# Optimization experiments

Hardware: AMD Instinct MI355X
Metric: run time of the kernel (lower is better)

## Reference

```python
import jax, jax.numpy as jnp
import numpy as np

DIM = 4096
N_HEADS = 32
N_KV_HEADS = 8
HEAD_DIM = DIM // N_HEADS  # 128
N_REP = N_HEADS // N_KV_HEADS  # 4
B, S = 1, 2048
ROPE_THETA = 500000.0


def setup_inputs() -> dict:
    key = jax.random.key(0)
    ks = jax.random.split(key, 5)
    sc = 0.02
    x = jax.random.normal(ks[0], (B, S, DIM), jnp.float32)
    wq = jax.random.normal(ks[1], (DIM, N_HEADS * HEAD_DIM), jnp.float32) * sc
    wk = jax.random.normal(ks[2], (DIM, N_KV_HEADS * HEAD_DIM), jnp.float32) * sc
    wv = jax.random.normal(ks[3], (DIM, N_KV_HEADS * HEAD_DIM), jnp.float32) * sc
    wo = jax.random.normal(ks[4], (N_HEADS * HEAD_DIM, DIM), jnp.float32) * sc
    # rotary frequencies: freqs_cis = exp(i * t * theta^(-2j/d)), j in [0, head_dim/2)
    inv_freq = 1.0 / (ROPE_THETA ** (jnp.arange(0, HEAD_DIM, 2, dtype=jnp.float32) / HEAD_DIM))
    t = jnp.arange(S, dtype=jnp.float32)
    ang = jnp.outer(t, inv_freq)  # (S, head_dim/2)
    freqs_cos = jnp.cos(ang)
    freqs_sin = jnp.sin(ang)
    # additive causal mask, broadcastable to (B, H, S, S)
    mask = jnp.where(jnp.triu(jnp.ones((S, S), bool), k=1), -jnp.inf, 0.0).astype(jnp.float32)[None, None]
    return {"x": x, "wq": wq, "wk": wk, "wv": wv, "wo": wo,
            "freqs_cos": freqs_cos, "freqs_sin": freqs_sin, "mask": mask}


def _apply_rotary(t, cos, sin):
    # t: (B, S, n, hd); complex multiply on consecutive pairs (x0,x1),(x2,x3),...
    b, s, n, hd = t.shape
    tr = t.reshape(b, s, n, hd // 2, 2)
    re, im = tr[..., 0], tr[..., 1]
    c = cos[None, :, None, :]
    sn = sin[None, :, None, :]
    out_re = re * c - im * sn
    out_im = re * sn + im * c
    return jnp.stack([out_re, out_im], axis=-1).reshape(b, s, n, hd)


def reference(x, wq, wk, wv, wo, freqs_cos, freqs_sin, mask):
    b, s, _ = x.shape
    xq = (x @ wq).reshape(b, s, N_HEADS, HEAD_DIM)
    xk = (x @ wk).reshape(b, s, N_KV_HEADS, HEAD_DIM)
    xv = (x @ wv).reshape(b, s, N_KV_HEADS, HEAD_DIM)
    xq = _apply_rotary(xq, freqs_cos, freqs_sin)
    xk = _apply_rotary(xk, freqs_cos, freqs_sin)
    # repeat_kv (GQA): expand kv heads to match query heads
    keys = jnp.repeat(xk, N_REP, axis=2)    # (b, s, H, hd)
    values = jnp.repeat(xv, N_REP, axis=2)
    # (b, H, s, hd)
    q = xq.transpose(0, 2, 1, 3)
    k = keys.transpose(0, 2, 1, 3)
    v = values.transpose(0, 2, 1, 3)
    scores = jnp.einsum('bhqd,bhkd->bhqk', q, k) / np.sqrt(HEAD_DIM).astype(np.float32)
    scores = scores + mask
    probs = jax.nn.softmax(scores.astype(jnp.float32), axis=-1).astype(q.dtype)
    out = jnp.einsum('bhqk,bhkd->bhqd', probs, v)
    out = out.transpose(0, 2, 1, 3).reshape(b, s, N_HEADS * HEAD_DIM)
    return out @ wo
```

## Files before the change

### kernel.cpp

```cpp
#include <hip/hip_runtime.h>
#include <cstdint>
#include <cstddef>

typedef _Float16 f16_t;
typedef f16_t f16x8 __attribute__((ext_vector_type(8)));
typedef float  floatx4 __attribute__((ext_vector_type(4)));

#define S_LEN 2048
#define DIM_  4096
#define NH    32
#define NKV   8
#define HD    128
#define KV_DIM (NKV * HD)
#define QLD   (DIM_ + 2 * KV_DIM)

__device__ __forceinline__ float bf16r(float x) {
    uint32_t u = __float_as_uint(x);
    u = (u + 0x7fffu + ((u >> 16) & 1u)) & 0xffff0000u;
    return __uint_as_float(u);
}

__device__ __forceinline__ void gload_lds16(const f16_t* g, f16_t* l) {
    __builtin_amdgcn_global_load_lds(
        (const __attribute__((address_space(1))) void*)g,
        (__attribute__((address_space(3))) void*)l, 16, 0, 0);
}

__global__ void f32_to_f16_kernel(const float* __restrict__ in,
                                  f16_t* __restrict__ out, int n) {
    int i = (blockIdx.x * blockDim.x + threadIdx.x) * 8;
    if (i >= n) return;
    float4 a = *(const float4*)(in + i);
    float4 b = *(const float4*)(in + i + 4);
    f16x8 o;
    o[0] = (f16_t)bf16r(a.x); o[1] = (f16_t)bf16r(a.y);
    o[2] = (f16_t)bf16r(a.z); o[3] = (f16_t)bf16r(a.w);
    o[4] = (f16_t)bf16r(b.x); o[5] = (f16_t)bf16r(b.y);
    o[6] = (f16_t)bf16r(b.z); o[7] = (f16_t)bf16r(b.w);
    *(f16x8*)(out + i) = o;
}

__global__ void transpose_weights_kernel(const float* __restrict__ wq,
                                         const float* __restrict__ wk,
                                         const float* __restrict__ wv,
                                         const float* __restrict__ wo,
                                         f16_t* __restrict__ wqkvT,
                                         f16_t* __restrict__ woT) {
    __shared__ float tile[32][33];
    int bid = blockIdx.x;
    const float* in; f16_t* out; int C;
    if (bid < 16384)      { in = wq; out = wqkvT;                          C = 4096; }
    else if (bid < 20480) { bid -= 16384; in = wk; out = wqkvT + (size_t)4096 * 4096; C = 1024; }
    else if (bid < 24576) { bid -= 20480; in = wv; out = wqkvT + (size_t)5120 * 4096; C = 1024; }
    else                  { bid -= 24576; in = wo; out = woT;              C = 4096; }
    int gpr = C / 32;
    int bx = (bid % gpr) * 32;
    int by = (bid / gpr) * 32;
    int tx = threadIdx.x, ty = threadIdx.y;
#pragma unroll
    for (int i = 0; i < 4; i++) {
        int r = ty + i * 8;
        tile[r][tx] = in[(size_t)(by + r) * C + bx + tx];
    }
    __syncthreads();
#pragma unroll
    for (int i = 0; i < 4; i++) {
        int r = ty + i * 8;
        out[(size_t)(bx + r) * 4096 + by + tx] = (f16_t)bf16r(tile[tx][r]);
    }
}

__global__ void transpose_f16_kernel(const f16_t* __restrict__ in,
                                     f16_t* __restrict__ out,
                                     int ldi, int ldo) {
    __shared__ float tile[32][33];
    int bx = blockIdx.x * 32;
    int by = blockIdx.y * 32;
    int tx = threadIdx.x, ty = threadIdx.y;
#pragma unroll
    for (int i = 0; i < 4; i++) {
        int r = ty + i * 8;
        tile[r][tx] = (float)in[(size_t)(by + r) * ldi + bx + tx];
    }
    __syncthreads();
#pragma unroll
    for (int i = 0; i < 4; i++) {
        int r = ty + i * 8;
        out[(size_t)(bx + r) * ldo + by + tx] = (f16_t)tile[tx][r];
    }
}

template <int BM, int BN, typename OutT>
__global__ __launch_bounds__(512) void gemm_pipe_kernel(
        const f16_t* __restrict__ A, const f16_t* __restrict__ BT,
        OutT* __restrict__ C, int M, int N, int K, int nbx) {
    constexpr int BK = 32;
    constexpr int WN = BN / 64;
    constexpr int WM = 8 / WN;
    constexpr int MT = BM / WM / 16;
    constexpr int NT = 4;
    constexpr int ABY = BM * BK * 2;
    constexpr int BBY = BN * BK * 2;
    constexpr int AISS = ABY / 8192;
    constexpr int BISS = BBY / 8192;
    constexpr int LOADS = AISS + BISS;
    constexpr int BUF_EL = (ABY + BBY) / 2;

    __shared__ f16_t lds[3 * BUF_EL];

    const int tid  = threadIdx.x;
    const int lane = tid & 63;
    const int wave = tid >> 6;
    const int quad = lane >> 4;
    const int l16  = lane & 15;
    const int wn = (wave % WN) * 64;
    const int wm = (wave / WN) * (BM / WM);

    const int nwg = gridDim.x;
    const int swz = (blockIdx.x & 7) * (nwg >> 3) + (blockIdx.x >> 3);
    const int m0 = (swz / nbx) * BM;
    const int n0 = (swz % nbx) * BN;

    const f16_t* Arow = A  + (size_t)m0 * K;
    const f16_t* Brow = BT + (size_t)n0 * K;
    const int nt_tiles = K / BK;

    floatx4 acc[MT][NT] = {};

    auto stage = [&](int t, int q) {
        const int k0 = t * BK;
        f16_t* LdA = lds + q * BUF_EL;
#pragma unroll
        for (int j = 0; j < AISS; j++) {
            int Lb  = j * 8192 + tid * 16;
            int row = Lb >> 6;
            int cb  = (Lb & 48) ^ (((Lb >> 7) & 3) << 4);
            gload_lds16(Arow + (size_t)row * K + k0 + (cb >> 1), LdA + (Lb >> 1));
        }
        f16_t* LdB = lds + q * BUF_EL + ABY / 2;
#pragma unroll
        for (int j = 0; j < BISS; j++) {
            int Lb  = j * 8192 + tid * 16;
            int row = Lb >> 6;
            int cb  = (Lb & 48) ^ (((Lb >> 7) & 3) << 4);
            gload_lds16(Brow + (size_t)row * K + k0 + (cb >> 1), LdB + (Lb >> 1));
        }
    };

    stage(0, 0);
    stage(1, 1);
    if constexpr (LOADS == 4) asm volatile("s_waitcnt vmcnt(4)" ::: "memory");
    else                      asm volatile("s_waitcnt vmcnt(3)" ::: "memory");
    __builtin_amdgcn_s_barrier();
    __builtin_amdgcn_sched_barrier(0);

    for (int t = 0; t < nt_tiles; ++t) {
        const int cur = t % 3;
        const bool pre = (t + 2 < nt_tiles);
        if (pre) stage(t + 2, (t + 2) % 3);

        const f16_t* Ab = lds + cur * BUF_EL;
        const f16_t* Bb = Ab + ABY / 2;
        f16x8 af[MT], bf[NT];
#pragma unroll
        for (int mt = 0; mt < MT; mt++) {
            int r  = wm + mt * 16 + l16;
            int cb = (quad * 16) ^ (((r >> 1) & 3) << 4);
            af[mt] = *(const f16x8*)(Ab + r * 32 + (cb >> 1));
        }
#pragma unroll
        for (int nt = 0; nt < NT; nt++) {
            int r  = wn + nt * 16 + l16;
            int cb = (quad * 16) ^ (((r >> 1) & 3) << 4);
            bf[nt] = *(const f16x8*)(Bb + r * 32 + (cb >> 1));
        }
        asm volatile("s_waitcnt lgkmcnt(0)" ::: "memory");
        __builtin_amdgcn_sched_barrier(0);
        __builtin_amdgcn_s_setprio(1);
#pragma unroll
        for (int mt = 0; mt < MT; mt++)
#pragma unroll
            for (int nt = 0; nt < NT; nt++)
                acc[mt][nt] = __builtin_amdgcn_mfma_f32_16x16x32_f16(
                    af[mt], bf[nt], acc[mt][nt], 0, 0, 0);
        __builtin_amdgcn_s_setprio(0);
        if (pre) {
            if constexpr (LOADS == 4) asm volatile("s_waitcnt vmcnt(4)" ::: "memory");
            else                      asm volatile("s_waitcnt vmcnt(3)" ::: "memory");
        } else {
            asm volatile("s_waitcnt vmcnt(0)" ::: "memory");
        }
        __builtin_amdgcn_s_barrier();
        __builtin_amdgcn_sched_barrier(0);
    }

#pragma unroll
    for (int mt = 0; mt < MT; mt++)
#pragma unroll
        for (int nt = 0; nt < NT; nt++)
#pragma unroll
            for (int rg = 0; rg < 4; rg++) {
                int row = m0 + wm + mt * 16 + quad * 4 + rg;
                int col = n0 + wn + nt * 16 + l16;
                C[(size_t)row * N + col] = (OutT)acc[mt][nt][rg];
            }
}

__global__ __launch_bounds__(512) void attn_kernel(
        const f16_t* __restrict__ QKV, const f16_t* __restrict__ Vt,
        const float* __restrict__ fcos, const float* __restrict__ fsin,
        f16_t* __restrict__ O) {
    constexpr int BK = 64;
    constexpr int KS = HD + 8;
    constexpr int VS = BK + 8;
    __shared__ f16_t Ks[BK][KS];
    __shared__ f16_t Vs[HD][VS];
    __shared__ f16_t Ps[8][16][72];

    const int tid  = threadIdx.x;
    const int lane = tid & 63;
    const int wave = tid >> 6;
    const int quad = lane >> 4;
    const int l16  = lane & 15;

    const int bid = blockIdx.x;
    const int h   = bid & 31;
    const int g   = bid >> 5;
    const int qt  = (g < 8) ? g : 23 - g;
    const int q0  = qt * 128;
    const int hkv = h >> 2;

    const int qrow = q0 + wave * 16 + l16;
    f16x8 qf[4];
    {
        const f16_t* Qg = QKV + (size_t)qrow * QLD + h * HD;
        const float* cr = fcos + qrow * 64;
        const float* sr = fsin + qrow * 64;
#pragma unroll
        for (int c = 0; c < 4; c++) {
            f16x8 v = *(const f16x8*)(Qg + c * 32 + quad * 8);
#pragma unroll
            for (int u = 0; u < 4; u++) {
                int fi = c * 16 + quad * 4 + u;
                float cc = bf16r(cr[fi]), ss = bf16r(sr[fi]);
                float re = (float)v[2 * u], im = (float)v[2 * u + 1];
                v[2 * u]     = (f16_t)(re * cc - im * ss);
                v[2 * u + 1] = (f16_t)(re * ss + im * cc);
            }
            qf[c] = v;
        }
    }

    floatx4 o_acc[8] = {};
    float m_run[4], l_run[4];
#pragma unroll
    for (int i = 0; i < 4; i++) { m_run[i] = -1e30f; l_run[i] = 0.f; }
    const float scale = 0.08838834764831845f;

    const int q_lo = q0 + wave * 16;
    const int q_hi = q_lo + 15;
    const int ntiles = q0 / BK + 2;

    const int krr = tid >> 4;
    const int kcc = (tid & 15) * 8;
    const int vr  = tid >> 3;
    const int vc  = (tid & 7) * 8;
    const f16_t* Vg = Vt + (size_t)hkv * HD * S_LEN;

    for (int t = 0; t < ntiles; t++) {
        const int k0 = t * BK;

#pragma unroll
        for (int p = 0; p < 2; p++) {
            int krow = k0 + p * 32 + krr;
            f16x8 v = *(const f16x8*)(QKV + (size_t)krow * QLD + DIM_ + hkv * HD + kcc);
            const float* cr = fcos + krow * 64;
            const float* sr = fsin + krow * 64;
#pragma unroll
            for (int u = 0; u < 4; u++) {
                int fi = kcc / 2 + u;
                float cc = bf16r(cr[fi]), ss = bf16r(sr[fi]);
                float re = (float)v[2 * u], im = (float)v[2 * u + 1];
                v[2 * u]     = (f16_t)(re * cc - im * ss);
                v[2 * u + 1] = (f16_t)(re * ss + im * cc);
            }
            *(f16x8*)&Ks[p * 32 + krr][kcc] = v;
        }
#pragma unroll
        for (int p = 0; p < 2; p++)
            *(f16x8*)&Vs[p * 64 + vr][vc] =
                *(const f16x8*)(Vg + (size_t)(p * 64 + vr) * S_LEN + k0 + vc);
        __syncthreads();

        if (k0 <= q_hi) {
            floatx4 sc4[4] = {};
#pragma unroll
            for (int nt = 0; nt < 4; nt++)
#pragma unroll
                for (int ks = 0; ks < 4; ks++) {
                    f16x8 kf = *(const f16x8*)&Ks[nt * 16 + l16][ks * 32 + quad * 8];
                    sc4[nt] = __builtin_amdgcn_mfma_f32_16x16x32_f16(qf[ks], kf, sc4[nt], 0, 0, 0);
                }

            const bool needmask = (k0 + BK - 1) > q_lo;
#pragma unroll
            for (int nt = 0; nt < 4; nt++)
#pragma unroll
                for (int rg = 0; rg < 4; rg++) {
                    float s = sc4[nt][rg] * scale;
                    if (needmask) {
                        int qg = q_lo + quad * 4 + rg;
                        int kg = k0 + nt * 16 + l16;
                        if (kg > qg) s = -1e30f;
                    }
                    sc4[nt][rg] = s;
                }

            float alpha[4];
#pragma unroll
            for (int rg = 0; rg < 4; rg++) {
                float m = fmaxf(fmaxf(sc4[0][rg], sc4[1][rg]), fmaxf(sc4[2][rg], sc4[3][rg]));
#pragma unroll
                for (int off = 8; off >= 1; off >>= 1)
                    m = fmaxf(m, __shfl_xor(m, off, 64));
                float mn = fmaxf(m_run[rg], m);
                alpha[rg] = __expf(m_run[rg] - mn);
                m_run[rg] = mn;
            }
            float rsum[4] = {0.f, 0.f, 0.f, 0.f};
#pragma unroll
            for (int nt = 0; nt < 4; nt++)
#pragma unroll
                for (int rg = 0; rg < 4; rg++) {
                    float p = __expf(sc4[nt][rg] - m_run[rg]);
                    sc4[nt][rg] = p;
                    rsum[rg] += p;
                }
#pragma unroll
            for (int rg = 0; rg < 4; rg++) {
                float s = rsum[rg];
#pragma unroll
                for (int off = 8; off >= 1; off >>= 1)
                    s += __shfl_xor(s, off, 64);
                l_run[rg] = l_run[rg] * alpha[rg] + s;
            }
#pragma unroll
            for (int dt = 0; dt < 8; dt++)
#pragma unroll
                for (int rg = 0; rg < 4; rg++) o_acc[dt][rg] *= alpha[rg];

#pragma unroll
            for (int nt = 0; nt < 4; nt++)
#pragma unroll
                for (int rg = 0; rg < 4; rg++)
                    Ps[wave][quad * 4 + rg][nt * 16 + l16] = (f16_t)sc4[nt][rg];
            asm volatile("s_waitcnt lgkmcnt(0)" ::: "memory");
            __builtin_amdgcn_sched_barrier(0);

#pragma unroll
            for (int ks = 0; ks < 2; ks++) {
                f16x8 pf = *(const f16x8*)&Ps[wave][l16][ks * 32 + quad * 8];
#pragma unroll
                for (int dt = 0; dt < 8; dt++) {
                    f16x8 vf = *(const f16x8*)&Vs[dt * 16 + l16][ks * 32 + quad * 8];
                    o_acc[dt] = __builtin_amdgcn_mfma_f32_16x16x32_f16(pf, vf, o_acc[dt], 0, 0, 0);
                }
            }
        }
        __syncthreads();
    }

#pragma unroll
    for (int rg = 0; rg < 4; rg++) {
        float inv_l = 1.0f / l_run[rg];
#pragma unroll
        for (int dt = 0; dt < 8; dt++) {
            int row = q0 + wave * 16 + quad * 4 + rg;
            int col = h * HD + dt * 16 + l16;
            O[(size_t)row * (NH * HD) + col] = (f16_t)(o_acc[dt][rg] * inv_l);
        }
    }
}

extern "C" void kernel_launch(void* const* d_in, const int* in_sizes, int n_in,
                              void* d_out, int out_size, void* d_ws, size_t ws_size,
                              hipStream_t stream) {
    const float* x    = (const float*)d_in[0];
    const float* wq   = (const float*)d_in[1];
    const float* wk   = (const float*)d_in[2];
    const float* wv   = (const float*)d_in[3];
    const float* wo   = (const float*)d_in[4];
    const float* fcos = (const float*)d_in[5];
    const float* fsin = (const float*)d_in[6];
    float* out = (float*)d_out;

    char* ws = (char*)d_ws;
    constexpr size_t MB = 1024 * 1024;
    f16_t* xb    = (f16_t*)(ws + 0 * MB);
    f16_t* wqkvT = (f16_t*)(ws + 16 * MB);
    f16_t* woT   = (f16_t*)(ws + 64 * MB);
    f16_t* QKVb  = (f16_t*)(ws + 96 * MB);
    f16_t* Vt    = (f16_t*)(ws + 120 * MB);
    f16_t* attnb = (f16_t*)(ws + 124 * MB);

    f32_to_f16_kernel<<<S_LEN * DIM_ / 8 / 256, 256, 0, stream>>>(x, xb, S_LEN * DIM_);
    transpose_weights_kernel<<<40960, dim3(32, 8), 0, stream>>>(wq, wk, wv, wo, wqkvT, woT);

    gemm_pipe_kernel<256, 256, f16_t><<<192, 512, 0, stream>>>(
        xb, wqkvT, QKVb, S_LEN, QLD, DIM_, QLD / 256);

    transpose_f16_kernel<<<dim3(KV_DIM / 32, S_LEN / 32), dim3(32, 8), 0, stream>>>(
        QKVb + 5120, Vt, QLD, S_LEN);

    attn_kernel<<<512, 512, 0, stream>>>(QKVb, Vt, fcos, fsin, attnb);

    gemm_pipe_kernel<256, 128, float><<<256, 512, 0, stream>>>(
        attnb, woT, out, S_LEN, DIM_, DIM_, DIM_ / 128);
}
```

Before: 561.9 us.

## Precompute RoPE in separate pass and streamline attention inner loop

Moves the rotary embedding and softmax scale out of the attention kernel into a standalone pass over the Q and K columns, so the attention loop no longer recomputes RoPE on K for every query tile. K and V tiles are now loaded with direct global-to-LDS loads into an XOR-swizzled layout. The loop rescales the accumulators only when the running max grows by more than a threshold, and computes the row sums with an MFMA against a ones vector instead of shuffle reductions. This adds a kernel launch and an extra read/write of Q and K, and pre-scaling Q and skipping rescales could slightly change fp16 precision.

```diff
diff --git a/kernel.cpp b/kernel.cpp
--- a/kernel.cpp
+++ b/kernel.cpp
@@ -90,6 +90,26 @@
     }
 }
 
+__global__ void rope_qk_kernel(f16_t* __restrict__ QKV,
+                               const float* __restrict__ fcos,
+                               const float* __restrict__ fsin) {
+    int c8 = (blockIdx.x * blockDim.x + threadIdx.x) * 8;
+    int row = blockIdx.y;
+    f16_t* p = QKV + (size_t)row * QLD + c8;
+    f16x8 v = *(f16x8*)p;
+    const float* cr = fcos + row * 64 + ((c8 & 127) >> 1);
+    const float* sr = fsin + row * 64 + ((c8 & 127) >> 1);
+    const float sc = (c8 < DIM_) ? 0.08838834764831845f : 1.0f;
+#pragma unroll
+    for (int u = 0; u < 4; u++) {
+        float cc = bf16r(cr[u]), ss = bf16r(sr[u]);
+        float re = (float)v[2 * u], im = (float)v[2 * u + 1];
+        v[2 * u]     = (f16_t)((re * cc - im * ss) * sc);
+        v[2 * u + 1] = (f16_t)((re * ss + im * cc) * sc);
+    }
+    *(f16x8*)p = v;
+}
+
 template <int BM, int BN, typename OutT>
 __global__ __launch_bounds__(512) void gemm_pipe_kernel(
         const f16_t* __restrict__ A, const f16_t* __restrict__ BT,
@@ -208,13 +228,10 @@
 
 __global__ __launch_bounds__(512) void attn_kernel(
         const f16_t* __restrict__ QKV, const f16_t* __restrict__ Vt,
-        const float* __restrict__ fcos, const float* __restrict__ fsin,
         f16_t* __restrict__ O) {
     constexpr int BK = 64;
-    constexpr int KS = HD + 8;
-    constexpr int VS = BK + 8;
-    __shared__ f16_t Ks[BK][KS];
-    __shared__ f16_t Vs[HD][VS];
+    __shared__ f16_t Ks[BK * HD];
+    __shared__ f16_t Vs[HD * BK];
     __shared__ f16_t Ps[8][16][72];
 
     const int tid  = threadIdx.x;
@@ -231,138 +248,113 @@
     const int hkv = h >> 2;
 
     const int qrow = q0 + wave * 16 + l16;
+    const f16_t* Qg = QKV + (size_t)qrow * QLD + h * HD;
     f16x8 qf[4];
-    {
-        const f16_t* Qg = QKV + (size_t)qrow * QLD + h * HD;
-        const float* cr = fcos + qrow * 64;
-        const float* sr = fsin + qrow * 64;
-#pragma unroll
-        for (int c = 0; c < 4; c++) {
-            f16x8 v = *(const f16x8*)(Qg + c * 32 + quad * 8);
-#pragma unroll
-            for (int u = 0; u < 4; u++) {
-                int fi = c * 16 + quad * 4 + u;
-                float cc = bf16r(cr[fi]), ss = bf16r(sr[fi]);
-                float re = (float)v[2 * u], im = (float)v[2 * u + 1];
-                v[2 * u]     = (f16_t)(re * cc - im * ss);
-                v[2 * u + 1] = (f16_t)(re * ss + im * cc);
-            }
-            qf[c] = v;
-        }
-    }
+#pragma unroll
+    for (int c = 0; c < 4; c++) qf[c] = *(const f16x8*)(Qg + c * 32 + quad * 8);
 
     floatx4 o_acc[8] = {};
-    float m_run[4], l_run[4];
-#pragma unroll
-    for (int i = 0; i < 4; i++) { m_run[i] = -1e30f; l_run[i] = 0.f; }
-    const float scale = 0.08838834764831845f;
+    floatx4 l_acc = {0.f, 0.f, 0.f, 0.f};
+    float m_run[4];
+#pragma unroll
+    for (int i = 0; i < 4; i++) m_run[i] = -1e30f;
+
+    f16x8 ones;
+#pragma unroll
+    for (int i = 0; i < 8; i++) ones[i] = (f16_t)1.0f;
 
     const int q_lo = q0 + wave * 16;
     const int q_hi = q_lo + 15;
     const int ntiles = q0 / BK + 2;
 
-    const int krr = tid >> 4;
-    const int kcc = (tid & 15) * 8;
-    const int vr  = tid >> 3;
-    const int vc  = (tid & 7) * 8;
-    const f16_t* Vg = Vt + (size_t)hkv * HD * S_LEN;
+    const int rK = tid >> 4;
+    const int cK = (((tid & 15) * 16) ^ ((rK & 7) << 4)) >> 1;
+    const f16_t* pK = QKV + (size_t)rK * QLD + DIM_ + hkv * HD + cK;
+    const int rV = tid >> 3;
+    const int cV = (((tid & 7) * 16) ^ ((rV & 7) << 4)) >> 1;
+    const f16_t* pV = Vt + (size_t)hkv * HD * S_LEN + (size_t)rV * S_LEN + cV;
+    f16_t* KsD0 = Ks + tid * 8;  f16_t* KsD1 = KsD0 + 4096;
+    f16_t* VsD0 = Vs + tid * 8;  f16_t* VsD1 = VsD0 + 4096;
 
     for (int t = 0; t < ntiles; t++) {
         const int k0 = t * BK;
 
-#pragma unroll
-        for (int p = 0; p < 2; p++) {
-            int krow = k0 + p * 32 + krr;
-            f16x8 v = *(const f16x8*)(QKV + (size_t)krow * QLD + DIM_ + hkv * HD + kcc);
-            const float* cr = fcos + krow * 64;
-            const float* sr = fsin + krow * 64;
-#pragma unroll
-            for (int u = 0; u < 4; u++) {
-                int fi = kcc / 2 + u;
-                float cc = bf16r(cr[fi]), ss = bf16r(sr[fi]);
-                float re = (float)v[2 * u], im = (float)v[2 * u + 1];
-                v[2 * u]     = (f16_t)(re * cc - im * ss);
-                v[2 * u + 1] = (f16_t)(re * ss + im * cc);
-            }
-            *(f16x8*)&Ks[p * 32 + krr][kcc] = v;
-        }
-#pragma unroll
-        for (int p = 0; p < 2; p++)
-            *(f16x8*)&Vs[p * 64 + vr][vc] =
-                *(const f16x8*)(Vg + (size_t)(p * 64 + vr) * S_LEN + k0 + vc);
+        gload_lds16(pK + (size_t)k0 * QLD, KsD0);
+        gload_lds16(pK + (size_t)(k0 + 32) * QLD, KsD1);
+        gload_lds16(pV + k0, VsD0);
+        gload_lds16(pV + k0 + (size_t)64 * S_LEN, VsD1);
+        asm volatile("s_waitcnt vmcnt(0)" ::: "memory");
         __syncthreads();
 
         if (k0 <= q_hi) {
             floatx4 sc4[4] = {};
 #pragma unroll
-            for (int nt = 0; nt < 4; nt++)
+            for (int nt = 0; nt < 4; nt++) {
+                const int r = nt * 16 + l16;
 #pragma unroll
                 for (int ks = 0; ks < 4; ks++) {
-                    f16x8 kf = *(const f16x8*)&Ks[nt * 16 + l16][ks * 32 + quad * 8];
+                    int cb = (ks * 64 + quad * 16) ^ ((r & 7) << 4);
+                    f16x8 kf = *(const f16x8*)(Ks + r * 128 + (cb >> 1));
                     sc4[nt] = __builtin_amdgcn_mfma_f32_16x16x32_f16(qf[ks], kf, sc4[nt], 0, 0, 0);
                 }
-
-            const bool needmask = (k0 + BK - 1) > q_lo;
-#pragma unroll
-            for (int nt = 0; nt < 4; nt++)
-#pragma unroll
-                for (int rg = 0; rg < 4; rg++) {
-                    float s = sc4[nt][rg] * scale;
-                    if (needmask) {
+            }
+
+            if ((k0 + BK - 1) > q_lo) {
+#pragma unroll
+                for (int nt = 0; nt < 4; nt++)
+#pragma unroll
+                    for (int rg = 0; rg < 4; rg++) {
                         int qg = q_lo + quad * 4 + rg;
                         int kg = k0 + nt * 16 + l16;
-                        if (kg > qg) s = -1e30f;
+                        if (kg > qg) sc4[nt][rg] = -1e30f;
                     }
-                    sc4[nt][rg] = s;
-                }
-
-            float alpha[4];
+            }
+
+            float m_t[4];
 #pragma unroll
             for (int rg = 0; rg < 4; rg++) {
                 float m = fmaxf(fmaxf(sc4[0][rg], sc4[1][rg]), fmaxf(sc4[2][rg], sc4[3][rg]));
 #pragma unroll
                 for (int off = 8; off >= 1; off >>= 1)
                     m = fmaxf(m, __shfl_xor(m, off, 64));
-                float mn = fmaxf(m_run[rg], m);
-                alpha[rg] = __expf(m_run[rg] - mn);
-                m_run[rg] = mn;
-            }
-            float rsum[4] = {0.f, 0.f, 0.f, 0.f};
+                m_t[rg] = m;
+            }
+            int grow = (m_t[0] > m_run[0] + 8.f) | (m_t[1] > m_run[1] + 8.f) |
+                       (m_t[2] > m_run[2] + 8.f) | (m_t[3] > m_run[3] + 8.f);
+            if (__any(grow)) {
+                float alpha[4];
+#pragma unroll
+                for (int rg = 0; rg < 4; rg++) {
+                    float mn = fmaxf(m_run[rg], m_t[rg]);
+                    alpha[rg] = __expf(m_run[rg] - mn);
+                    m_run[rg] = mn;
+                }
+#pragma unroll
+                for (int dt = 0; dt < 8; dt++)
+#pragma unroll
+                    for (int rg = 0; rg < 4; rg++) o_acc[dt][rg] *= alpha[rg];
+#pragma unroll
+                for (int rg = 0; rg < 4; rg++) l_acc[rg] *= alpha[rg];
+            }
+
 #pragma unroll
             for (int nt = 0; nt < 4; nt++)
 #pragma unroll
-                for (int rg = 0; rg < 4; rg++) {
-                    float p = __expf(sc4[nt][rg] - m_run[rg]);
-                    sc4[nt][rg] = p;
-                    rsum[rg] += p;
-                }
-#pragma unroll
-            for (int rg = 0; rg < 4; rg++) {
-                float s = rsum[rg];
-#pragma unroll
-                for (int off = 8; off >= 1; off >>= 1)
-                    s += __shfl_xor(s, off, 64);
-                l_run[rg] = l_run[rg] * alpha[rg] + s;
-            }
-#pragma unroll
-            for (int dt = 0; dt < 8; dt++)
-#pragma unroll
-                for (int rg = 0; rg < 4; rg++) o_acc[dt][rg] *= alpha[rg];
-
-#pragma unroll
-            for (int nt = 0; nt < 4; nt++)
-#pragma unroll
                 for (int rg = 0; rg < 4; rg++)
-                    Ps[wave][quad * 4 + rg][nt * 16 + l16] = (f16_t)sc4[nt][rg];
+                    Ps[wave][quad * 4 + rg][nt * 16 + l16] =
+                        (f16_t)__expf(sc4[nt][rg] - m_run[rg]);
             asm volatile("s_waitcnt lgkmcnt(0)" ::: "memory");
             __builtin_amdgcn_sched_barrier(0);
 
 #pragma unroll
             for (int ks = 0; ks < 2; ks++) {
                 f16x8 pf = *(const f16x8*)&Ps[wave][l16][ks * 32 + quad * 8];
+                l_acc = __builtin_amdgcn_mfma_f32_16x16x32_f16(pf, ones, l_acc, 0, 0, 0);
 #pragma unroll
                 for (int dt = 0; dt < 8; dt++) {
-                    f16x8 vf = *(const f16x8*)&Vs[dt * 16 + l16][ks * 32 + quad * 8];
+                    const int r = dt * 16 + l16;
+                    int cb = (ks * 64 + quad * 16) ^ ((r & 7) << 4);
+                    f16x8 vf = *(const f16x8*)(Vs + r * 64 + (cb >> 1));
                     o_acc[dt] = __builtin_amdgcn_mfma_f32_16x16x32_f16(pf, vf, o_acc[dt], 0, 0, 0);
                 }
             }
@@ -372,7 +364,7 @@
 
 #pragma unroll
     for (int rg = 0; rg < 4; rg++) {
-        float inv_l = 1.0f / l_run[rg];
+        float inv_l = 1.0f / l_acc[rg];
 #pragma unroll
         for (int dt = 0; dt < 8; dt++) {
             int row = q0 + wave * 16 + quad * 4 + rg;
@@ -409,10 +401,11 @@
     gemm_pipe_kernel<256, 256, f16_t><<<192, 512, 0, stream>>>(
         xb, wqkvT, QKVb, S_LEN, QLD, DIM_, QLD / 256);
 
+    rope_qk_kernel<<<dim3(5, S_LEN), 128, 0, stream>>>(QKVb, fcos, fsin);
     transpose_f16_kernel<<<dim3(KV_DIM / 32, S_LEN / 32), dim3(32, 8), 0, stream>>>(
         QKVb + 5120, Vt, QLD, S_LEN);
 
-    attn_kernel<<<512, 512, 0, stream>>>(QKVb, Vt, fcos, fsin, attnb);
+    attn_kernel<<<512, 512, 0, stream>>>(QKVb, Vt, attnb);
 
     gemm_pipe_kernel<256, 128, float><<<256, 512, 0, stream>>>(
         attnb, woT, out, S_LEN, DIM_, DIM_, DIM_ / 128);
```

Result: faster. 522.1 us (-7.1%).
